# Kernel optimization log

Hardware: AMD Instinct MI355X
Metric: run time of the kernel (lower is better)

The kernel has to match this reference:

```python
import jax, jax.numpy as jnp
import numpy as np

D_IN = 128
HID = 32
HEADS = 8
OUT = 16
N = 50000
E = 400000
NEG_SLOPE = 0.2


def setup_inputs() -> dict:
    key = jax.random.key(0)
    ks = jax.random.split(key, 12)
    s = lambda k, sh: jax.random.normal(k, sh, dtype=jnp.float32) * 0.05
    return {
        "x": jax.random.normal(ks[0], (N, D_IN), dtype=jnp.float32),
        "edge_index": jax.random.randint(ks[1], (2, E), 0, N, dtype=jnp.int64),
        # conv_1: GATv2, heads=8, concat=True
        "W1l": s(ks[2], (D_IN, HEADS * HID)),
        "W1r": s(ks[3], (D_IN, HEADS * HID)),
        "att1": s(ks[4], (HEADS, HID)),
        "b1": jnp.zeros((HEADS * HID,), dtype=jnp.float32),
        # conv_2: GATv2, heads=1, concat=False
        "W2l": s(ks[5], (HEADS * HID, HID)),
        "W2r": s(ks[6], (HEADS * HID, HID)),
        "att2": s(ks[7], (1, HID)),
        "b2": jnp.zeros((HID,), dtype=jnp.float32),
        # final linear
        "Wlin": s(ks[8], (HID, OUT)),
        "blin": jnp.zeros((OUT,), dtype=jnp.float32),
    }


def _gatv2(x, src, dst, Wl, Wr, att, bias, n_nodes):
    heads, ch = att.shape
    xl = (x @ Wl).reshape(n_nodes, heads, ch)   # source-side transform
    xr = (x @ Wr).reshape(n_nodes, heads, ch)   # target-side transform
    # per-edge GATv2 score: a^T leaky_relu(xl_i + xr_j)
    e = jax.nn.leaky_relu(xl[src] + xr[dst], NEG_SLOPE)        # [E,H,C]
    logits = jnp.einsum('ehc,hc->eh', e, att)                  # [E,H]
    # segment softmax grouped by destination node
    m = jax.ops.segment_max(logits, dst, num_segments=n_nodes)
    m = jnp.where(jnp.isfinite(m), m, 0.0)
    p = jnp.exp(logits - m[dst])
    denom = jax.ops.segment_sum(p, dst, num_segments=n_nodes)
    alpha = p / jnp.maximum(denom[dst], 1e-16)                 # [E,H]
    # scatter-sum aggregation of weighted source features
    out = jax.ops.segment_sum(alpha[:, :, None] * xl[src], dst, num_segments=n_nodes)
    return out + bias.reshape(1, heads, ch)                    # [N,H,C]


def reference(x, edge_index, W1l, W1r, att1, b1, W2l, W2r, att2, b2, Wlin, blin):
    n = x.shape[0]
    loops = jnp.arange(n, dtype=edge_index.dtype)
    ei = jnp.concatenate([edge_index, jnp.stack([loops, loops])], axis=1)  # add_self_loops=True
    src, dst = ei[0], ei[1]

    h = _gatv2(x, src, dst, W1l, W1r, att1, b1, n)   # [N,8,32]
    h = jax.nn.elu(h.reshape(n, -1))                  # concat=True; dropout=identity (eval)

    h = _gatv2(h, src, dst, W2l, W2r, att2, b2, n)   # [N,1,32]
    h = jax.nn.elu(h[:, 0, :])                        # concat=False, heads=1 -> mean == squeeze

    return h @ Wlin + blin                            # [N,16]
```

## Files before the change

kernel.cpp:

```cpp
#include <hip/hip_runtime.h>
#include <cstdint>
#include <cstddef>

#define N_NODES 50000
#define N_EDGES 400000
#define E_TOT   (N_EDGES + N_NODES)
#define D_INF   128
#define C1      256
#define HIDC    32
#define OUTC    16
#define NEG_SLOPE 0.2f
#define LOG2E   1.44269504088896340736f
#define SCAN_B  ((N_NODES + 1023) / 1024)

typedef __bf16 bf16x8 __attribute__((ext_vector_type(8)));
typedef float  floatx4 __attribute__((ext_vector_type(4)));
typedef float  floatx2 __attribute__((ext_vector_type(2)));
typedef unsigned int uintx4 __attribute__((ext_vector_type(4)));
typedef unsigned int uintx2 __attribute__((ext_vector_type(2)));
typedef unsigned short ushortx8 __attribute__((ext_vector_type(8)));
typedef unsigned short ushortx4 __attribute__((ext_vector_type(4)));

__device__ __forceinline__ unsigned short f2bf(float f) {
  unsigned int u = __builtin_bit_cast(unsigned int, f);
  u += 0x7FFFu + ((u >> 16) & 1u);
  return (unsigned short)(u >> 16);
}
__device__ __forceinline__ float bf2f(unsigned short u) {
  return __builtin_bit_cast(float, (unsigned int)u << 16);
}
__device__ __forceinline__ floatx2 bf2x2(unsigned int u) {
  floatx2 r;
  r.x = __builtin_bit_cast(float, u << 16);
  r.y = __builtin_bit_cast(float, u & 0xffff0000u);
  return r;
}

__global__ void k_detect(const int* __restrict__ ei, int* __restrict__ flag) {
  __shared__ int s;
  if (threadIdx.x == 0) s = 0;
  __syncthreads();
  atomicOr(&s, ei[2 * threadIdx.x + 1]);
  __syncthreads();
  if (threadIdx.x == 0) *flag = (s == 0) ? 1 : 0;
}
__device__ __forceinline__ int ld_src(const int* ei, int f, int e) {
  return f ? ei[2 * e] : ei[e];
}
__device__ __forceinline__ int ld_dst(const int* ei, int f, int e) {
  return f ? ei[2 * (N_EDGES + e)] : ei[N_EDGES + e];
}

__global__ void k_transpose(const float* __restrict__ in,
                            unsigned short* __restrict__ out, int R, int C) {
  int i = blockIdx.x * 256 + threadIdx.x;
  if (i < R * C) {
    int r = i / C, c = i % C;
    out[c * R + r] = f2bf(in[i]);
  }
}

__global__ void k_deg(const int* __restrict__ ei, const int* __restrict__ flag,
                      int* __restrict__ deg) {
  int e = blockIdx.x * 256 + threadIdx.x;
  if (e < E_TOT) {
    int dst = (e < N_EDGES) ? ld_dst(ei, *flag, e) : (e - N_EDGES);
    if ((unsigned)dst < N_NODES) atomicAdd(&deg[dst], 1);
  }
}

__global__ __launch_bounds__(1024) void k_scan_blk(
    const int* __restrict__ deg, int* __restrict__ incl,
    int* __restrict__ bsum, int n) {
  __shared__ int sbuf[1024];
  const int t = threadIdx.x;
  const int i = blockIdx.x * 1024 + t;
  const int v = (i < n) ? deg[i] : 0;
  sbuf[t] = v;
  __syncthreads();
  for (int off = 1; off < 1024; off <<= 1) {
    int add = (t >= off) ? sbuf[t - off] : 0;
    __syncthreads();
    sbuf[t] += add;
    __syncthreads();
  }
  if (i < n) incl[i] = sbuf[t];
  if (t == 1023) bsum[blockIdx.x] = sbuf[1023];
}

__global__ void k_scan_top(int* __restrict__ bsum, int* __restrict__ rowptr,
                           int nb) {
  const int lane = threadIdx.x;
  const int v = (lane < nb) ? bsum[lane] : 0;
  int incl = v;
#pragma unroll
  for (int off = 1; off < 64; off <<= 1) {
    int t = __shfl_up(incl, off);
    if (lane >= off) incl += t;
  }
  if (lane < nb) bsum[lane] = incl - v;
  if (lane == 63) rowptr[N_NODES] = incl;
}

__global__ __launch_bounds__(1024) void k_scan_add(
    const int* __restrict__ deg, const int* __restrict__ incl,
    const int* __restrict__ bsum, int* __restrict__ rowptr,
    int* __restrict__ cursor, int n) {
  const int i = blockIdx.x * 1024 + threadIdx.x;
  if (i < n) {
    const int e = bsum[blockIdx.x] + incl[i] - deg[i];
    rowptr[i] = e;
    cursor[i] = e;
  }
}

__global__ void k_fill(const int* __restrict__ ei, const int* __restrict__ flag,
                       int* __restrict__ cursor, int* __restrict__ esrc) {
  int e = blockIdx.x * 256 + threadIdx.x;
  if (e < E_TOT) {
    int src, dst;
    if (e < N_EDGES) { src = ld_src(ei, *flag, e); dst = ld_dst(ei, *flag, e); }
    else             { src = dst = e - N_EDGES; }
    if ((unsigned)src < N_NODES && (unsigned)dst < N_NODES) {
      int pos = atomicAdd(&cursor[dst], 1);
      esrc[pos] = src;
    }
  }
}

__device__ __forceinline__ bf16x8 load8(const unsigned short* p) {
  uintx4 raw = *reinterpret_cast<const uintx4*>(p);
  return __builtin_bit_cast(bf16x8, raw);
}
__device__ __forceinline__ bf16x8 load8(const float* p) {
  floatx4 a = *reinterpret_cast<const floatx4*>(p);
  floatx4 b = *reinterpret_cast<const floatx4*>(p + 4);
  ushortx8 u;
#pragma unroll
  for (int i = 0; i < 4; ++i) { u[i] = f2bf(a[i]); u[4 + i] = f2bf(b[i]); }
  return __builtin_bit_cast(bf16x8, u);
}

template <int K, int NCOLS, typename AT>
__global__ __launch_bounds__(256) void k_gemm_dual(
    const AT* __restrict__ A,
    const unsigned short* __restrict__ BT0, const unsigned short* __restrict__ BT1,
    unsigned short* __restrict__ C0, unsigned short* __restrict__ C1_, int M) {
  const int wave = threadIdx.x >> 6;
  const int lane = threadIdx.x & 63;
  const int lo = lane & 15;
  const int q  = lane >> 4;
  const int unit = blockIdx.x * 4 + wave;
  const int r0 = unit * 32;
  if (r0 >= M) return;
  const bool two = (r0 + 16) < M;
  constexpr int KB = K / 32;

  bf16x8 afrag[2][KB];
#pragma unroll
  for (int kb = 0; kb < KB; ++kb)
    afrag[0][kb] = load8(A + (size_t)(r0 + lo) * K + kb * 32 + q * 8);
  if (two) {
#pragma unroll
    for (int kb = 0; kb < KB; ++kb)
      afrag[1][kb] = load8(A + (size_t)(r0 + 16 + lo) * K + kb * 32 + q * 8);
  }

#pragma unroll
  for (int o = 0; o < 2; ++o) {
    const unsigned short* BT = o ? BT1 : BT0;
    unsigned short* C = o ? C1_ : C0;
#pragma unroll
    for (int nt = 0; nt < NCOLS / 16; ++nt) {
      floatx4 acc0 = {0.f, 0.f, 0.f, 0.f};
      floatx4 acc1 = {0.f, 0.f, 0.f, 0.f};
      const unsigned short* bptr = BT + (size_t)(nt * 16 + lo) * K + q * 8;
#pragma unroll
      for (int kb = 0; kb < KB; ++kb) {
        bf16x8 b = load8(bptr + kb * 32);
        acc0 = __builtin_amdgcn_mfma_f32_16x16x32_bf16(afrag[0][kb], b, acc0, 0, 0, 0);
        if (two)
          acc1 = __builtin_amdgcn_mfma_f32_16x16x32_bf16(afrag[1][kb], b, acc1, 0, 0, 0);
      }
#pragma unroll
      for (int r = 0; r < 4; ++r) {
        C[(size_t)(r0 + q * 4 + r) * NCOLS + nt * 16 + lo] = f2bf(acc0[r]);
        if (two)
          C[(size_t)(r0 + 16 + q * 4 + r) * NCOLS + nt * 16 + lo] = f2bf(acc1[r]);
      }
    }
  }
}

__global__ __launch_bounds__(256) void k_gat1(
    const unsigned short* __restrict__ xl1, const unsigned short* __restrict__ xr1,
    const float* __restrict__ att1, const float* __restrict__ b1,
    const int* __restrict__ rowptr, const int* __restrict__ esrc,
    unsigned short* __restrict__ h1) {
  const int wave = threadIdx.x >> 6;
  const int lane = threadIdx.x & 63;
  const int dst = blockIdx.x * 4 + wave;
  if (dst >= N_NODES) return;
  const int h = lane >> 5;
  const int w = lane & 31;
  const int cb = w * 8;

  floatx2 xr2v[4], att2v[4];
  {
    uintx4 r = *reinterpret_cast<const uintx4*>(xr1 + (size_t)dst * C1 + cb);
    floatx4 a0 = *reinterpret_cast<const floatx4*>(att1 + cb);
    floatx4 a1 = *reinterpret_cast<const floatx4*>(att1 + cb + 4);
#pragma unroll
    for (int j = 0; j < 4; ++j) xr2v[j] = bf2x2(r[j]);
    att2v[0] = floatx2{a0.x, a0.y} * LOG2E;
    att2v[1] = floatx2{a0.z, a0.w} * LOG2E;
    att2v[2] = floatx2{a1.x, a1.y} * LOG2E;
    att2v[3] = floatx2{a1.z, a1.w} * LOG2E;
  }

  const int beg = rowptr[dst], end = rowptr[dst + 1];
  const int n = end - beg;
  const int* ep = esrc + beg;

  float l = 0.f;
  floatx2 acc2[4] = {{0.f, 0.f}, {0.f, 0.f}, {0.f, 0.f}, {0.f, 0.f}};

  auto process = [&](uintx4 cur) {
    floatx2 xs2[4];
    floatx2 v2 = {0.f, 0.f};
#pragma unroll
    for (int j = 0; j < 4; ++j) {
      xs2[j] = bf2x2(cur[j]);
      floatx2 s2 = xs2[j] + xr2v[j];
      floatx2 e2 = __builtin_elementwise_max(s2, s2 * NEG_SLOPE);
      v2 = __builtin_elementwise_fma(e2, att2v[j], v2);
    }
    float v = v2.x + v2.y;
    v += __shfl_xor(v, 1);
    v += __shfl_xor(v, 2);
    v = fminf(fmaxf(v, -100.f), 100.f);
    const float p = __builtin_amdgcn_exp2f(v);
    l += p;
    const floatx2 p2 = {p, p};
#pragma unroll
    for (int j = 0; j < 4; ++j)
      acc2[j] = __builtin_elementwise_fma(p2, xs2[j], acc2[j]);
  };

  uintx4 bufa = {0u, 0u, 0u, 0u}, bufb = {0u, 0u, 0u, 0u};
  if (h < n)
    bufa = *reinterpret_cast<const uintx4*>(xl1 + (size_t)ep[h] * C1 + cb);
  if (h + 2 < n)
    bufb = *reinterpret_cast<const uintx4*>(xl1 + (size_t)ep[h + 2] * C1 + cb);
  int i = h;
  while (i < n) {
    process(bufa);
    if (i + 4 < n)
      bufa = *reinterpret_cast<const uintx4*>(xl1 + (size_t)ep[i + 4] * C1 + cb);
    i += 2;
    if (i >= n) break;
    process(bufb);
    if (i + 4 < n)
      bufb = *reinterpret_cast<const uintx4*>(xl1 + (size_t)ep[i + 4] * C1 + cb);
    i += 2;
  }

  l += __shfl_xor(l, 32);
#pragma unroll
  for (int j = 0; j < 4; ++j) {
    acc2[j].x += __shfl_xor(acc2[j].x, 32);
    acc2[j].y += __shfl_xor(acc2[j].y, 32);
  }

  if (h == 0) {
    const float inv = 1.f / fmaxf(l, 1e-16f);
    ushortx8 ob;
#pragma unroll
    for (int j = 0; j < 4; ++j) {
      float z0 = acc2[j].x * inv + b1[cb + 2 * j];
      float z1 = acc2[j].y * inv + b1[cb + 2 * j + 1];
      z0 = z0 > 0.f ? z0 : (__expf(z0) - 1.f);
      z1 = z1 > 0.f ? z1 : (__expf(z1) - 1.f);
      ob[2 * j]     = f2bf(z0);
      ob[2 * j + 1] = f2bf(z1);
    }
    *reinterpret_cast<ushortx8*>(h1 + (size_t)dst * C1 + cb) = ob;
  }
}

__global__ __launch_bounds__(256) void k_gat2(
    const unsigned short* __restrict__ xl2, const unsigned short* __restrict__ xr2,
    const float* __restrict__ att2, const float* __restrict__ b2,
    const float* __restrict__ Wlin, const float* __restrict__ blin,
    const int* __restrict__ rowptr, const int* __restrict__ esrc,
    float* __restrict__ out) {
  __shared__ float sh[4][32];
  const int wave = threadIdx.x >> 6;
  const int lane = threadIdx.x & 63;
  const int dst = blockIdx.x * 4 + wave;
  if (dst >= N_NODES) return;
  const int o8 = lane >> 3;
  const int w = lane & 7;
  const int cb = w * 4;

  floatx2 xr2v[2], att2v[2];
  {
    uintx2 r = *reinterpret_cast<const uintx2*>(xr2 + (size_t)dst * HIDC + cb);
    floatx4 a = *reinterpret_cast<const floatx4*>(att2 + cb);
    xr2v[0] = bf2x2(r[0]);
    xr2v[1] = bf2x2(r[1]);
    att2v[0] = floatx2{a.x, a.y} * LOG2E;
    att2v[1] = floatx2{a.z, a.w} * LOG2E;
  }

  const int beg = rowptr[dst], end = rowptr[dst + 1];
  const int n = end - beg;
  const int* ep = esrc + beg;

  float l = 0.f;
  floatx2 acc2[2] = {{0.f, 0.f}, {0.f, 0.f}};

  auto process = [&](uintx2 cur) {
    floatx2 xs2[2];
    floatx2 v2 = {0.f, 0.f};
#pragma unroll
    for (int j = 0; j < 2; ++j) {
      xs2[j] = bf2x2(cur[j]);
      floatx2 s2 = xs2[j] + xr2v[j];
      floatx2 e2 = __builtin_elementwise_max(s2, s2 * NEG_SLOPE);
      v2 = __builtin_elementwise_fma(e2, att2v[j], v2);
    }
    float v = v2.x + v2.y;
    v += __shfl_xor(v, 1);
    v += __shfl_xor(v, 2);
    v += __shfl_xor(v, 4);
    v = fminf(fmaxf(v, -100.f), 100.f);
    const float p = __builtin_amdgcn_exp2f(v);
    l += p;
    const floatx2 p2 = {p, p};
#pragma unroll
    for (int j = 0; j < 2; ++j)
      acc2[j] = __builtin_elementwise_fma(p2, xs2[j], acc2[j]);
  };

  uintx2 bufa = {0u, 0u}, bufb = {0u, 0u};
  if (o8 < n)
    bufa = *reinterpret_cast<const uintx2*>(xl2 + (size_t)ep[o8] * HIDC + cb);
  if (o8 + 8 < n)
    bufb = *reinterpret_cast<const uintx2*>(xl2 + (size_t)ep[o8 + 8] * HIDC + cb);
  int i = o8;
  while (i < n) {
    process(bufa);
    if (i + 16 < n)
      bufa = *reinterpret_cast<const uintx2*>(xl2 + (size_t)ep[i + 16] * HIDC + cb);
    i += 8;
    if (i >= n) break;
    process(bufb);
    if (i + 16 < n)
      bufb = *reinterpret_cast<const uintx2*>(xl2 + (size_t)ep[i + 16] * HIDC + cb);
    i += 8;
  }

#pragma unroll
  for (int k = 8; k < 64; k <<= 1) {
    l += __shfl_xor(l, k);
#pragma unroll
    for (int j = 0; j < 2; ++j) {
      acc2[j].x += __shfl_xor(acc2[j].x, k);
      acc2[j].y += __shfl_xor(acc2[j].y, k);
    }
  }

  if (o8 == 0) {
    const float inv = 1.f / fmaxf(l, 1e-16f);
#pragma unroll
    for (int j = 0; j < 2; ++j) {
      float z0 = acc2[j].x * inv + b2[cb + 2 * j];
      float z1 = acc2[j].y * inv + b2[cb + 2 * j + 1];
      z0 = z0 > 0.f ? z0 : (__expf(z0) - 1.f);
      z1 = z1 > 0.f ? z1 : (__expf(z1) - 1.f);
      sh[wave][cb + 2 * j]     = z0;
      sh[wave][cb + 2 * j + 1] = z1;
    }
  }
  if (lane < OUTC) {
    float o = blin[lane];
#pragma unroll
    for (int k = 0; k < 32; ++k)
      o = fmaf(sh[wave][k], Wlin[k * OUTC + lane], o);
    out[(size_t)dst * OUTC + lane] = o;
  }
}

static inline int cdiv(int a, int b) { return (a + b - 1) / b; }

extern "C" void kernel_launch(void* const* d_in, const int* in_sizes, int n_in,
                              void* d_out, int out_size, void* d_ws, size_t ws_size,
                              hipStream_t stream) {
  const float* x    = (const float*)d_in[0];
  const int*   ei   = (const int*)d_in[1];
  const float* W1l  = (const float*)d_in[2];
  const float* W1r  = (const float*)d_in[3];
  const float* att1 = (const float*)d_in[4];
  const float* b1   = (const float*)d_in[5];
  const float* W2l  = (const float*)d_in[6];
  const float* W2r  = (const float*)d_in[7];
  const float* att2 = (const float*)d_in[8];
  const float* b2   = (const float*)d_in[9];
  const float* Wlin = (const float*)d_in[10];
  const float* blin = (const float*)d_in[11];
  float* out = (float*)d_out;

  char* w = (char*)d_ws;
  auto alloc = [&](size_t bytes) -> char* {
    char* p = w;
    w += (bytes + 255) & ~(size_t)255;
    return p;
  };
  char* regionA = alloc((size_t)N_NODES * C1 * 2);
  unsigned short* xl1 = (unsigned short*)regionA;
  unsigned short* xl2 = (unsigned short*)regionA;
  unsigned short* xr2 = (unsigned short*)(regionA + (size_t)N_NODES * HIDC * 2 + 256);
  unsigned short* xr1 = (unsigned short*)alloc((size_t)N_NODES * C1 * 2);
  unsigned short* h1  = xr1;
  unsigned short* W1lT = (unsigned short*)alloc((size_t)D_INF * C1 * 2);
  unsigned short* W1rT = (unsigned short*)alloc((size_t)D_INF * C1 * 2);
  unsigned short* W2lT = (unsigned short*)alloc((size_t)C1 * HIDC * 2);
  unsigned short* W2rT = (unsigned short*)alloc((size_t)C1 * HIDC * 2);
  int* rowptr = (int*)alloc((size_t)(N_NODES + 1) * 4);
  int* cursor = (int*)alloc((size_t)N_NODES * 4);
  int* deg    = (int*)alloc((size_t)N_NODES * 4);
  int* incl   = (int*)alloc((size_t)N_NODES * 4);
  int* bsum   = (int*)alloc((size_t)SCAN_B * 4);
  int* esrc   = (int*)alloc((size_t)E_TOT * 4);
  int* flag   = (int*)alloc(4);

  hipMemsetAsync(deg, 0, (size_t)N_NODES * 4, stream);
  k_detect<<<1, 64, 0, stream>>>(ei, flag);

  k_transpose<<<cdiv(D_INF * C1, 256), 256, 0, stream>>>(W1l, W1lT, D_INF, C1);
  k_transpose<<<cdiv(D_INF * C1, 256), 256, 0, stream>>>(W1r, W1rT, D_INF, C1);
  k_transpose<<<cdiv(C1 * HIDC, 256), 256, 0, stream>>>(W2l, W2lT, C1, HIDC);
  k_transpose<<<cdiv(C1 * HIDC, 256), 256, 0, stream>>>(W2r, W2rT, C1, HIDC);

  k_deg<<<cdiv(E_TOT, 256), 256, 0, stream>>>(ei, flag, deg);
  k_scan_blk<<<SCAN_B, 1024, 0, stream>>>(deg, incl, bsum, N_NODES);
  k_scan_top<<<1, 64, 0, stream>>>(bsum, rowptr, SCAN_B);
  k_scan_add<<<SCAN_B, 1024, 0, stream>>>(deg, incl, bsum, rowptr, cursor, N_NODES);
  k_fill<<<cdiv(E_TOT, 256), 256, 0, stream>>>(ei, flag, cursor, esrc);

  const int gblocks = cdiv(cdiv(N_NODES, 32), 4);

  k_gemm_dual<D_INF, C1><<<gblocks, 256, 0, stream>>>(x, W1lT, W1rT, xl1, xr1, N_NODES);

  k_gat1<<<cdiv(N_NODES, 4), 256, 0, stream>>>(xl1, xr1, att1, b1, rowptr, esrc, h1);

  k_gemm_dual<C1, HIDC><<<gblocks, 256, 0, stream>>>(h1, W2lT, W2rT, xl2, xr2, N_NODES);

  k_gat2<<<cdiv(N_NODES, 4), 256, 0, stream>>>(xl2, xr2, att2, b2, Wlin, blin,
                                               rowptr, esrc, out);
}
```

Before: 270.3 us.

## Merge preprocessing launches, replace scan with atomic allocation, overlap fill with GEMM

```diff
diff --git a/kernel.cpp b/kernel.cpp
--- a/kernel.cpp
+++ b/kernel.cpp
@@ -11,11 +11,20 @@
 #define OUTC    16
 #define NEG_SLOPE 0.2f
 #define LOG2E   1.44269504088896340736f
-#define SCAN_B  ((N_NODES + 1023) / 1024)
+
+#define ESRC_CAP (E_TOT + 3 * N_NODES + 16)
+
+#define ZB_DEG ((N_NODES + 255) / 256)
+#define ZB_ESR ((ESRC_CAP + 255) / 256)
+#define TB_W   ((2 * D_INF * C1 + 2 * C1 * HIDC + 255) / 256)
+#define PREP_GRID (ZB_DEG + ZB_ESR + TB_W + 1)
+
+#define FILLB ((E_TOT + 255) / 256)
 
 typedef __bf16 bf16x8 __attribute__((ext_vector_type(8)));
 typedef float  floatx4 __attribute__((ext_vector_type(4)));
 typedef float  floatx2 __attribute__((ext_vector_type(2)));
+typedef int    intx4  __attribute__((ext_vector_type(4)));
 typedef unsigned int uintx4 __attribute__((ext_vector_type(4)));
 typedef unsigned int uintx2 __attribute__((ext_vector_type(2)));
 typedef unsigned short ushortx8 __attribute__((ext_vector_type(8)));
@@ -36,14 +45,6 @@
   return r;
 }
 
-__global__ void k_detect(const int* __restrict__ ei, int* __restrict__ flag) {
-  __shared__ int s;
-  if (threadIdx.x == 0) s = 0;
-  __syncthreads();
-  atomicOr(&s, ei[2 * threadIdx.x + 1]);
-  __syncthreads();
-  if (threadIdx.x == 0) *flag = (s == 0) ? 1 : 0;
-}
 __device__ __forceinline__ int ld_src(const int* ei, int f, int e) {
   return f ? ei[2 * e] : ei[e];
 }
@@ -51,13 +52,53 @@
   return f ? ei[2 * (N_EDGES + e)] : ei[N_EDGES + e];
 }
 
-__global__ void k_transpose(const float* __restrict__ in,
-                            unsigned short* __restrict__ out, int R, int C) {
-  int i = blockIdx.x * 256 + threadIdx.x;
-  if (i < R * C) {
-    int r = i / C, c = i % C;
-    out[c * R + r] = f2bf(in[i]);
-  }
+__global__ __launch_bounds__(256) void k_prep(
+    const int* __restrict__ ei,
+    const float* __restrict__ W1l, const float* __restrict__ W1r,
+    const float* __restrict__ W2l, const float* __restrict__ W2r,
+    unsigned short* __restrict__ W1lT, unsigned short* __restrict__ W1rT,
+    unsigned short* __restrict__ W2lT, unsigned short* __restrict__ W2rT,
+    int* __restrict__ deg, int* __restrict__ esrc,
+    int* __restrict__ total, int* __restrict__ flag) {
+  __shared__ int sdet;
+  const int bid = blockIdx.x;
+  const int tid = threadIdx.x;
+  if (bid < ZB_DEG) {
+    const int i = bid * 256 + tid;
+    if (i < N_NODES) deg[i] = 0;
+    if (bid == 0 && tid == 0) *total = 0;
+    return;
+  }
+  if (bid < ZB_DEG + ZB_ESR) {
+    const int i = (bid - ZB_DEG) * 256 + tid;
+    if (i < ESRC_CAP) esrc[i] = 0;
+    return;
+  }
+  if (bid < ZB_DEG + ZB_ESR + TB_W) {
+    int idx = (bid - ZB_DEG - ZB_ESR) * 256 + tid;
+    if (idx < D_INF * C1) {
+      const int r = idx >> 8, c = idx & 255;
+      W1lT[c * D_INF + r] = f2bf(W1l[idx]);
+    } else if (idx < 2 * D_INF * C1) {
+      idx -= D_INF * C1;
+      const int r = idx >> 8, c = idx & 255;
+      W1rT[c * D_INF + r] = f2bf(W1r[idx]);
+    } else if (idx < 2 * D_INF * C1 + C1 * HIDC) {
+      idx -= 2 * D_INF * C1;
+      const int r = idx >> 5, c = idx & 31;
+      W2lT[c * C1 + r] = f2bf(W2l[idx]);
+    } else {
+      idx -= 2 * D_INF * C1 + C1 * HIDC;
+      const int r = idx >> 5, c = idx & 31;
+      W2rT[c * C1 + r] = f2bf(W2r[idx]);
+    }
+    return;
+  }
+  if (tid == 0) sdet = 0;
+  __syncthreads();
+  if (tid < 64) atomicOr(&sdet, ei[2 * tid + 1]);
+  __syncthreads();
+  if (tid == 0) *flag = (sdet == 0) ? 1 : 0;
 }
 
 __global__ void k_deg(const int* __restrict__ ei, const int* __restrict__ flag,
@@ -69,62 +110,27 @@
   }
 }
 
-__global__ __launch_bounds__(1024) void k_scan_blk(
-    const int* __restrict__ deg, int* __restrict__ incl,
-    int* __restrict__ bsum, int n) {
-  __shared__ int sbuf[1024];
-  const int t = threadIdx.x;
-  const int i = blockIdx.x * 1024 + t;
-  const int v = (i < n) ? deg[i] : 0;
-  sbuf[t] = v;
-  __syncthreads();
-  for (int off = 1; off < 1024; off <<= 1) {
-    int add = (t >= off) ? sbuf[t - off] : 0;
-    __syncthreads();
-    sbuf[t] += add;
-    __syncthreads();
-  }
-  if (i < n) incl[i] = sbuf[t];
-  if (t == 1023) bsum[blockIdx.x] = sbuf[1023];
-}
-
-__global__ void k_scan_top(int* __restrict__ bsum, int* __restrict__ rowptr,
-                           int nb) {
-  const int lane = threadIdx.x;
-  const int v = (lane < nb) ? bsum[lane] : 0;
-  int incl = v;
+__global__ __launch_bounds__(256) void k_alloc(
+    const int* __restrict__ deg, int* __restrict__ rowptr,
+    int* __restrict__ cursor, int* __restrict__ total) {
+  const int i = blockIdx.x * 256 + threadIdx.x;
+  const int lane = threadIdx.x & 63;
+  const int d  = (i < N_NODES) ? deg[i] : 0;
+  const int d4 = (d + 3) & ~3;
+  int incl = d4;
 #pragma unroll
   for (int off = 1; off < 64; off <<= 1) {
     int t = __shfl_up(incl, off);
     if (lane >= off) incl += t;
   }
-  if (lane < nb) bsum[lane] = incl - v;
-  if (lane == 63) rowptr[N_NODES] = incl;
-}
-
-__global__ __launch_bounds__(1024) void k_scan_add(
-    const int* __restrict__ deg, const int* __restrict__ incl,
-    const int* __restrict__ bsum, int* __restrict__ rowptr,
-    int* __restrict__ cursor, int n) {
-  const int i = blockIdx.x * 1024 + threadIdx.x;
-  if (i < n) {
-    const int e = bsum[blockIdx.x] + incl[i] - deg[i];
+  const int wtot = __shfl(incl, 63);
+  int wb = 0;
+  if (lane == 63) wb = atomicAdd(total, wtot);
+  wb = __shfl(wb, 63);
+  if (i < N_NODES) {
+    const int e = wb + incl - d4;
     rowptr[i] = e;
     cursor[i] = e;
-  }
-}
-
-__global__ void k_fill(const int* __restrict__ ei, const int* __restrict__ flag,
-                       int* __restrict__ cursor, int* __restrict__ esrc) {
-  int e = blockIdx.x * 256 + threadIdx.x;
-  if (e < E_TOT) {
-    int src, dst;
-    if (e < N_EDGES) { src = ld_src(ei, *flag, e); dst = ld_dst(ei, *flag, e); }
-    else             { src = dst = e - N_EDGES; }
-    if ((unsigned)src < N_NODES && (unsigned)dst < N_NODES) {
-      int pos = atomicAdd(&cursor[dst], 1);
-      esrc[pos] = src;
-    }
   }
 }
 
@@ -142,15 +148,12 @@
 }
 
 template <int K, int NCOLS, typename AT>
-__global__ __launch_bounds__(256) void k_gemm_dual(
-    const AT* __restrict__ A,
+__device__ __forceinline__ void gemm_dual_body(
+    int unit, int lane, const AT* __restrict__ A,
     const unsigned short* __restrict__ BT0, const unsigned short* __restrict__ BT1,
     unsigned short* __restrict__ C0, unsigned short* __restrict__ C1_, int M) {
-  const int wave = threadIdx.x >> 6;
-  const int lane = threadIdx.x & 63;
   const int lo = lane & 15;
   const int q  = lane >> 4;
-  const int unit = blockIdx.x * 4 + wave;
   const int r0 = unit * 32;
   if (r0 >= M) return;
   const bool two = (r0 + 16) < M;
@@ -192,11 +195,46 @@
   }
 }
 
+__global__ __launch_bounds__(256) void k_fill_gemm1(
+    const int* __restrict__ ei, const int* __restrict__ flag,
+    int* __restrict__ cursor, int* __restrict__ esrc,
+    const float* __restrict__ A,
+    const unsigned short* __restrict__ BT0, const unsigned short* __restrict__ BT1,
+    unsigned short* __restrict__ C0, unsigned short* __restrict__ C1_) {
+  if (blockIdx.x < FILLB) {
+    const int e = blockIdx.x * 256 + threadIdx.x;
+    if (e < E_TOT) {
+      int src, dst;
+      if (e < N_EDGES) { src = ld_src(ei, *flag, e); dst = ld_dst(ei, *flag, e); }
+      else             { src = dst = e - N_EDGES; }
+      if ((unsigned)src < N_NODES && (unsigned)dst < N_NODES) {
+        int pos = atomicAdd(&cursor[dst], 1);
+        esrc[pos] = src;
+      }
+    }
+    return;
+  }
+  const int wave = threadIdx.x >> 6;
+  const int lane = threadIdx.x & 63;
+  gemm_dual_body<D_INF, C1, float>((blockIdx.x - FILLB) * 4 + wave, lane,
+                                   A, BT0, BT1, C0, C1_, N_NODES);
+}
+
+__global__ __launch_bounds__(256) void k_gemm2(
+    const unsigned short* __restrict__ A,
+    const unsigned short* __restrict__ BT0, const unsigned short* __restrict__ BT1,
+    unsigned short* __restrict__ C0, unsigned short* __restrict__ C1_) {
+  const int wave = threadIdx.x >> 6;
+  const int lane = threadIdx.x & 63;
+  gemm_dual_body<C1, HIDC, unsigned short>(blockIdx.x * 4 + wave, lane,
+                                           A, BT0, BT1, C0, C1_, N_NODES);
+}
+
 __global__ __launch_bounds__(256) void k_gat1(
     const unsigned short* __restrict__ xl1, const unsigned short* __restrict__ xr1,
     const float* __restrict__ att1, const float* __restrict__ b1,
-    const int* __restrict__ rowptr, const int* __restrict__ esrc,
-    unsigned short* __restrict__ h1) {
+    const int* __restrict__ rowptr, const int* __restrict__ deg,
+    const int* __restrict__ esrc, unsigned short* __restrict__ h1) {
   const int wave = threadIdx.x >> 6;
   const int lane = threadIdx.x & 63;
   const int dst = blockIdx.x * 4 + wave;
@@ -204,6 +242,11 @@
   const int h = lane >> 5;
   const int w = lane & 31;
   const int cb = w * 8;
+  const unsigned short* __restrict__ xb = xl1 + cb;
+
+  const int beg = rowptr[dst];
+  const int n   = deg[dst];
+  const int* __restrict__ ep = esrc + beg;
 
   floatx2 xr2v[4], att2v[4];
   {
@@ -218,14 +261,14 @@
     att2v[3] = floatx2{a1.z, a1.w} * LOG2E;
   }
 
-  const int beg = rowptr[dst], end = rowptr[dst + 1];
-  const int n = end - beg;
-  const int* ep = esrc + beg;
-
   float l = 0.f;
   floatx2 acc2[4] = {{0.f, 0.f}, {0.f, 0.f}, {0.f, 0.f}, {0.f, 0.f}};
 
-  auto process = [&](uintx4 cur) {
+  auto gath = [&](int a, int b) {
+    const int s = h ? b : a;
+    return *reinterpret_cast<const uintx4*>(xb + (size_t)s * C1);
+  };
+  auto process = [&](uintx4 cur, float keep) {
     floatx2 xs2[4];
     floatx2 v2 = {0.f, 0.f};
 #pragma unroll
@@ -238,8 +281,8 @@
     float v = v2.x + v2.y;
     v += __shfl_xor(v, 1);
     v += __shfl_xor(v, 2);
-    v = fminf(fmaxf(v, -100.f), 100.f);
-    const float p = __builtin_amdgcn_exp2f(v);
+    v = __builtin_amdgcn_fmed3f(v, -100.f, 100.f);
+    const float p = __builtin_amdgcn_exp2f(v) * keep;
     l += p;
     const floatx2 p2 = {p, p};
 #pragma unroll
@@ -247,22 +290,44 @@
       acc2[j] = __builtin_elementwise_fma(p2, xs2[j], acc2[j]);
   };
 
-  uintx4 bufa = {0u, 0u, 0u, 0u}, bufb = {0u, 0u, 0u, 0u};
-  if (h < n)
-    bufa = *reinterpret_cast<const uintx4*>(xl1 + (size_t)ep[h] * C1 + cb);
-  if (h + 2 < n)
-    bufb = *reinterpret_cast<const uintx4*>(xl1 + (size_t)ep[h + 2] * C1 + cb);
-  int i = h;
-  while (i < n) {
-    process(bufa);
-    if (i + 4 < n)
-      bufa = *reinterpret_cast<const uintx4*>(xl1 + (size_t)ep[i + 4] * C1 + cb);
-    i += 2;
-    if (i >= n) break;
-    process(bufb);
-    if (i + 4 < n)
-      bufb = *reinterpret_cast<const uintx4*>(xl1 + (size_t)ep[i + 4] * C1 + cb);
-    i += 2;
+  intx4 ja = *reinterpret_cast<const intx4*>(ep);
+  intx4 jb = *reinterpret_cast<const intx4*>(ep + 4);
+  uintx4 g0 = {0u,0u,0u,0u}, g1 = {0u,0u,0u,0u}, g2 = {0u,0u,0u,0u}, g3 = {0u,0u,0u,0u};
+  if (h     < n) g0 = gath(ja.x, ja.y);
+  if (h + 2 < n) g1 = gath(ja.z, ja.w);
+  if (h + 4 < n) g2 = gath(jb.x, jb.y);
+  if (h + 6 < n) g3 = gath(jb.z, jb.w);
+  intx4 na = *reinterpret_cast<const intx4*>(ep + 8);
+  intx4 nb = *reinterpret_cast<const intx4*>(ep + 12);
+
+  int base = 0;
+  while (true) {
+    const int rem = n - base;
+    const bool more = rem > 8;
+    uintx4 t0, t1, t2, t3;
+    intx4 ma, mb;
+    if (more) {
+      const int remn = rem - 8;
+      t0 = t1 = t2 = t3 = uintx4{0u,0u,0u,0u};
+      if (h     < remn) t0 = gath(na.x, na.y);
+      if (h + 2 < remn) t1 = gath(na.z, na.w);
+      if (h + 4 < remn) t2 = gath(nb.x, nb.y);
+      if (h + 6 < remn) t3 = gath(nb.z, nb.w);
+      ma = *reinterpret_cast<const intx4*>(ep + base + 16);
+      mb = *reinterpret_cast<const intx4*>(ep + base + 20);
+    }
+    if (rem >= 8) {
+      process(g0, 1.f); process(g1, 1.f); process(g2, 1.f); process(g3, 1.f);
+    } else {
+      process(g0, (h     < rem) ? 1.f : 0.f);
+      process(g1, (h + 2 < rem) ? 1.f : 0.f);
+      process(g2, (h + 4 < rem) ? 1.f : 0.f);
+      process(g3, (h + 6 < rem) ? 1.f : 0.f);
+    }
+    if (!more) break;
+    g0 = t0; g1 = t1; g2 = t2; g3 = t3;
+    na = ma; nb = mb;
+    base += 8;
   }
 
   l += __shfl_xor(l, 32);
@@ -292,8 +357,8 @@
     const unsigned short* __restrict__ xl2, const unsigned short* __restrict__ xr2,
     const float* __restrict__ att2, const float* __restrict__ b2,
     const float* __restrict__ Wlin, const float* __restrict__ blin,
-    const int* __restrict__ rowptr, const int* __restrict__ esrc,
-    float* __restrict__ out) {
+    const int* __restrict__ rowptr, const int* __restrict__ deg,
+    const int* __restrict__ esrc, float* __restrict__ out) {
   __shared__ float sh[4][32];
   const int wave = threadIdx.x >> 6;
   const int lane = threadIdx.x & 63;
@@ -313,9 +378,9 @@
     att2v[1] = floatx2{a.z, a.w} * LOG2E;
   }
 
-  const int beg = rowptr[dst], end = rowptr[dst + 1];
-  const int n = end - beg;
-  const int* ep = esrc + beg;
+  const int beg = rowptr[dst];
+  const int n   = deg[dst];
+  const int* __restrict__ ep = esrc + beg;
 
   float l = 0.f;
   floatx2 acc2[2] = {{0.f, 0.f}, {0.f, 0.f}};
@@ -334,7 +399,7 @@
     v += __shfl_xor(v, 1);
     v += __shfl_xor(v, 2);
     v += __shfl_xor(v, 4);
-    v = fminf(fmaxf(v, -100.f), 100.f);
+    v = __builtin_amdgcn_fmed3f(v, -100.f, 100.f);
     const float p = __builtin_amdgcn_exp2f(v);
     l += p;
     const floatx2 p2 = {p, p};
@@ -427,36 +492,29 @@
   unsigned short* W1rT = (unsigned short*)alloc((size_t)D_INF * C1 * 2);
   unsigned short* W2lT = (unsigned short*)alloc((size_t)C1 * HIDC * 2);
   unsigned short* W2rT = (unsigned short*)alloc((size_t)C1 * HIDC * 2);
-  int* rowptr = (int*)alloc((size_t)(N_NODES + 1) * 4);
+  int* rowptr = (int*)alloc((size_t)N_NODES * 4);
   int* cursor = (int*)alloc((size_t)N_NODES * 4);
   int* deg    = (int*)alloc((size_t)N_NODES * 4);
-  int* incl   = (int*)alloc((size_t)N_NODES * 4);
-  int* bsum   = (int*)alloc((size_t)SCAN_B * 4);
-  int* esrc   = (int*)alloc((size_t)E_TOT * 4);
+  int* esrc   = (int*)alloc((size_t)ESRC_CAP * 4);
   int* flag   = (int*)alloc(4);
-
-  hipMemsetAsync(deg, 0, (size_t)N_NODES * 4, stream);
-  k_detect<<<1, 64, 0, stream>>>(ei, flag);
-
-  k_transpose<<<cdiv(D_INF * C1, 256), 256, 0, stream>>>(W1l, W1lT, D_INF, C1);
-  k_transpose<<<cdiv(D_INF * C1, 256), 256, 0, stream>>>(W1r, W1rT, D_INF, C1);
-  k_transpose<<<cdiv(C1 * HIDC, 256), 256, 0, stream>>>(W2l, W2lT, C1, HIDC);
-  k_transpose<<<cdiv(C1 * HIDC, 256), 256, 0, stream>>>(W2r, W2rT, C1, HIDC);
-
+  int* total  = (int*)alloc(4);
+
+  k_prep<<<PREP_GRID, 256, 0, stream>>>(ei, W1l, W1r, W2l, W2r,
+                                        W1lT, W1rT, W2lT, W2rT,
+                                        deg, esrc, total, flag);
   k_deg<<<cdiv(E_TOT, 256), 256, 0, stream>>>(ei, flag, deg);
-  k_scan_blk<<<SCAN_B, 1024, 0, stream>>>(deg, incl, bsum, N_NODES);
-  k_scan_top<<<1, 64, 0, stream>>>(bsum, rowptr, SCAN_B);
-  k_scan_add<<<SCAN_B, 1024, 0, stream>>>(deg, incl, bsum, rowptr, cursor, N_NODES);
-  k_fill<<<cdiv(E_TOT, 256), 256, 0, stream>>>(ei, flag, cursor, esrc);
+  k_alloc<<<cdiv(N_NODES, 256), 256, 0, stream>>>(deg, rowptr, cursor, total);
 
   const int gblocks = cdiv(cdiv(N_NODES, 32), 4);
 
-  k_gemm_dual<D_INF, C1><<<gblocks, 256, 0, stream>>>(x, W1lT, W1rT, xl1, xr1, N_NODES);
-
-  k_gat1<<<cdiv(N_NODES, 4), 256, 0, stream>>>(xl1, xr1, att1, b1, rowptr, esrc, h1);
-
-  k_gemm_dual<C1, HIDC><<<gblocks, 256, 0, stream>>>(h1, W2lT, W2rT, xl2, xr2, N_NODES);
+  k_fill_gemm1<<<FILLB + gblocks, 256, 0, stream>>>(ei, flag, cursor, esrc,
+                                                    x, W1lT, W1rT, xl1, xr1);
+
+  k_gat1<<<cdiv(N_NODES, 4), 256, 0, stream>>>(xl1, xr1, att1, b1,
+                                               rowptr, deg, esrc, h1);
+
+  k_gemm2<<<gblocks, 256, 0, stream>>>(h1, W2lT, W2rT, xl2, xr2);
 
   k_gat2<<<cdiv(N_NODES, 4), 256, 0, stream>>>(xl2, xr2, att2, b2, Wlin, blin,
-                                               rowptr, esrc, out);
-}
+                                               rowptr, deg, esrc, out);
+}
```

Result: slower. 310.1 us (+14.7%).
